# Performance work log

Measured on AMD Instinct MI355X. Metric: run time of the kernel, lower is better.

Reference implementation:

```python
import jax, jax.numpy as jnp
import numpy as np

ANGSTROM_TO_METER = 1e-10
COULOMB_CONSTANT = 8987551792.3
ELECTRON_CHARGE = 1.602176634e-19
EV_TO_JOULE = 1.602176634e-19
COUL_DAMPING_BETA = 18.7
R0_METER = 2.2 * ANGSTROM_TO_METER
EWALD_P = 0.3275911
EWALD_A = (0.254829592, -0.284496736, 1.421413741, -1.453152027, 1.061405429)
EWALD_F = 2.0

N_ATOMS = 200000
N_EDGES = 8000000
N_GRAPHS = 256


def setup_inputs() -> dict:
    key = jax.random.key(0)
    k1, k2, k3, k4, k5 = jax.random.split(key, 5)
    dij = jax.random.normal(k1, (N_EDGES, 3), dtype=jnp.float32)  # Angstrom
    pred_charge = jax.random.normal(k2, (N_ATOMS,), dtype=jnp.float32)  # e
    g_ewald = jnp.full((1,), 3.0e9, dtype=jnp.float32)  # 1/m (~0.3 1/A)
    row = jax.random.randint(k3, (N_EDGES,), 0, N_ATOMS)
    col = jax.random.randint(k4, (N_EDGES,), 0, N_ATOMS)
    batch = jnp.sort(jax.random.randint(k5, (N_ATOMS,), 0, N_GRAPHS))
    return {"dij": dij, "pred_charge": pred_charge, "g_ewald": g_ewald,
            "row": row, "col": col, "batch": batch}


def reference(dij, pred_charge, g_ewald, row, col, batch):
    n_atoms = pred_charge.shape[0]
    dij_m = dij * ANGSTROM_TO_METER                      # [E,3] meters
    rij = jnp.sqrt(jnp.sum(dij_m * dij_m, axis=-1))      # [E]
    q = pred_charge * ELECTRON_CHARGE                    # Coulombs
    prefactor = COULOMB_CONSTANT * q[row] * q[col] / rij
    # exponential short-range damping below r0
    damp = jnp.where(rij < R0_METER,
                     jnp.exp(-COUL_DAMPING_BETA * (R0_METER - rij) / R0_METER),
                     jnp.ones_like(rij))
    ecoul = 0.5 * prefactor * damp
    fcoul = prefactor * damp / rij
    # Ewald real-space correction via Abramowitz-Stegun erfc polynomial
    grij = g_ewald[0] * rij
    expm2 = jnp.exp(-grij * grij)
    t = 1.0 / (1.0 + EWALD_P * grij)
    a0, a1, a2, a3, a4 = EWALD_A
    erfc = t * (a0 + t * (a1 + t * (a2 + t * (a3 + t * a4)))) * expm2
    ecoul = ecoul + prefactor * (erfc - 1.0)
    fcoul = fcoul + prefactor * (erfc + EWALD_F * grij * expm2 - 1.0) / rij
    # per-edge force vector, converted J/m -> eV/A
    fij = dij_m * (fcoul / rij)[:, None]                 # [E,3]
    fij_ev = fij * ANGSTROM_TO_METER / EV_TO_JOULE
    ecoul_ev = ecoul / EV_TO_JOULE
    # scatter edge->atom (by row), then atom->molecule (by batch)
    e_atom = jax.ops.segment_sum(ecoul_ev, row, num_segments=n_atoms)
    coul_energy = jax.ops.segment_sum(e_atom, batch, num_segments=N_GRAPHS)
    force_row = jax.ops.segment_sum(fij_ev, row, num_segments=n_atoms)
    force_col = jax.ops.segment_sum(fij_ev, col, num_segments=n_atoms)
    coul_force = force_row - force_col
    return coul_energy, coul_force
```

## Files before the change

kernel.cpp:

```cpp
#include <hip/hip_runtime.h>
#include <hip/hip_fp16.h>

#define N_GRAPHS_C 256
#define CHUNK_LOG 12
#define CHUNK (1 << CHUNK_LOG)
#define MAXB 64
#define NSLICE 12
#define NSLICE_FB 10
#define TPA 256
#define TPBB 512
#define SD 64
#define PSTR (CHUNK + 8)
#define FP_SCALE 1024.0f
#define FP_INV   (1.0f / 1024.0f)

__device__ __forceinline__ void edge_math(
    float dx, float dy, float dz, float qr, float qc, float gA,
    float& fx, float& fy, float& fz, float& ecoul)
{
    const float KEV = (float)(8987551792.3 * 1.602176634e-9);
    float r2 = dx * dx + dy * dy + dz * dz;
    float inv_r = rsqrtf(r2);
    float rA = r2 * inv_r;

    float pref = KEV * qr * qc * inv_r;

    float damp = 1.0f;
    if (rA < 2.2f)
        damp = __expf(-18.7f * (2.2f - rA) * (1.0f / 2.2f));

    float grij = gA * rA;
    float expm2 = __expf(-grij * grij);
    float t = 1.0f / (1.0f + 0.3275911f * grij);
    float erfc = t * (0.254829592f +
                 t * (-0.284496736f +
                 t * (1.421413741f +
                 t * (-1.453152027f +
                 t * 1.061405429f)))) * expm2;

    ecoul = pref * (0.5f * damp + (erfc - 1.0f));
    float S = damp + erfc + 2.0f * grij * expm2 - 1.0f;
    float fs = pref * S * (inv_r * inv_r);
    fx = dx * fs; fy = dy * fs; fz = dz * fs;
}

__device__ __forceinline__ uint2 pack_rec(float fx, float fy, float fz, unsigned lid)
{
    uint2 u;
    u.x = __builtin_bit_cast(unsigned, __floats2half2_rn(fx, fy));
    u.y = (__builtin_bit_cast(unsigned, __floats2half2_rn(fz, 0.0f)) & 0xFFFFu) |
          (lid << 16);
    return u;
}

__device__ __forceinline__ void acc_rec(int* acc, unsigned w0, unsigned w1)
{
    float2 xy = __half22float2(__builtin_bit_cast(__half2, w0));
    float fz = __half2float(__builtin_bit_cast(__half2, w1).x);
    unsigned idx = w1 >> 16;
    atomicAdd(&acc[idx],            __float2int_rn(xy.x * FP_SCALE));
    atomicAdd(&acc[PSTR + idx],     __float2int_rn(xy.y * FP_SCALE));
    atomicAdd(&acc[2 * PSTR + idx], __float2int_rn(fz   * FP_SCALE));
}

__global__ __launch_bounds__(256) void prep_qg(
    const float* __restrict__ q, const int* __restrict__ batch,
    float2* __restrict__ qg, float* __restrict__ ovf, int n_atoms)
{
    int i = blockIdx.x * 256 + threadIdx.x;
    if (i < n_atoms) {
        qg[i] = make_float2(q[i], __int_as_float(batch[i]));
        ovf[3 * i + 0] = 0.f;
        ovf[3 * i + 1] = 0.f;
        ovf[3 * i + 2] = 0.f;
    }
}

__global__ __launch_bounds__(TPA) void passA(
    const float* __restrict__ dij, const float2* __restrict__ qg,
    const float* __restrict__ g_ewald,
    const int* __restrict__ row, const int* __restrict__ col,
    uint2* __restrict__ records, int cap,
    unsigned* __restrict__ cnt_table,
    float* __restrict__ e_part,
    float* __restrict__ ovf,
    int n_edges, int nb, int tile_g)
{
    __shared__ uint2    stage[MAXB][SD + 1];
    __shared__ unsigned scnt[MAXB];
    __shared__ unsigned cnt[MAXB];
    __shared__ float    e_graph[4 * N_GRAPHS_C];

    int tid  = threadIdx.x;
    int wid  = tid >> 6;
    int lane = tid & 63;
    if (tid < MAXB) { scnt[tid] = 0u; cnt[tid] = 0u; }
    for (int i = tid; i < 4 * N_GRAPHS_C; i += TPA) e_graph[i] = 0.f;
    __syncthreads();

    float* e_my = &e_graph[wid * N_GRAPHS_C];

    int n4 = n_edges >> 2;
    int gbase = blockIdx.x * tile_g;
    int g1 = min(gbase + tile_g, n4);
    int nph = tile_g / TPA;

    const int4* row4 = (const int4*)row;
    const int4* col4 = (const int4*)col;
    const float4* dij4 = (const float4*)dij;

    const float gA = g_ewald[0] * 1e-10f;
    size_t blk_base = (size_t)blockIdx.x * nb * cap;

    int4 r_cur = make_int4(0, 0, 0, 0), c_cur = make_int4(0, 0, 0, 0);
    float2 vr_cur[4], vc_cur[4];
    {
        int g = gbase + tid;
        if (g < g1) { r_cur = row4[g]; c_cur = col4[g]; }
        vr_cur[0] = qg[r_cur.x]; vc_cur[0] = qg[c_cur.x];
        vr_cur[1] = qg[r_cur.y]; vc_cur[1] = qg[c_cur.y];
        vr_cur[2] = qg[r_cur.z]; vc_cur[2] = qg[c_cur.z];
        vr_cur[3] = qg[r_cur.w]; vc_cur[3] = qg[c_cur.w];
    }

    for (int p = 0; p < nph; ++p) {
        int g = gbase + p * TPA + tid;

        int4 r_nxt = make_int4(0, 0, 0, 0), c_nxt = make_int4(0, 0, 0, 0);
        if (p + 1 < nph && g + TPA < g1) {
            r_nxt = row4[g + TPA]; c_nxt = col4[g + TPA];
        }

        if (g < g1) {
            float4 d0 = dij4[3 * g + 0];
            float4 d1 = dij4[3 * g + 1];
            float4 d2 = dij4[3 * g + 2];
            float ex[4] = {d0.x, d0.w, d1.z, d2.y};
            float ey[4] = {d0.y, d1.x, d1.w, d2.z};
            float ez[4] = {d0.z, d1.y, d2.x, d2.w};
            int rr[4] = {r_cur.x, r_cur.y, r_cur.z, r_cur.w};
            int cc[4] = {c_cur.x, c_cur.y, c_cur.z, c_cur.w};

            #pragma unroll
            for (int j = 0; j < 4; ++j) {
                int r = rr[j], c = cc[j];
                float fx, fy, fz, ec;
                edge_math(ex[j], ey[j], ez[j], vr_cur[j].x, vc_cur[j].x, gA,
                          fx, fy, fz, ec);

                atomicAdd(&e_my[__float_as_int(vr_cur[j].y)], ec);

                int br = r >> CHUNK_LOG, bc = c >> CHUNK_LOG;
                unsigned pr = atomicAdd(&scnt[br], 1u);
                unsigned pc = atomicAdd(&scnt[bc], 1u);
                if (pr < SD)
                    stage[br][pr] = pack_rec(fx, fy, fz, (unsigned)(r & (CHUNK - 1)));
                else {
                    atomicAdd(&ovf[3 * r + 0], fx);
                    atomicAdd(&ovf[3 * r + 1], fy);
                    atomicAdd(&ovf[3 * r + 2], fz);
                }
                if (pc < SD)
                    stage[bc][pc] = pack_rec(-fx, -fy, -fz, (unsigned)(c & (CHUNK - 1)));
                else {
                    atomicAdd(&ovf[3 * c + 0], -fx);
                    atomicAdd(&ovf[3 * c + 1], -fy);
                    atomicAdd(&ovf[3 * c + 2], -fz);
                }
            }
        }

        float2 vr_n[4], vc_n[4];
        vr_n[0] = qg[r_nxt.x]; vc_n[0] = qg[c_nxt.x];
        vr_n[1] = qg[r_nxt.y]; vc_n[1] = qg[c_nxt.y];
        vr_n[2] = qg[r_nxt.z]; vc_n[2] = qg[c_nxt.z];
        vr_n[3] = qg[r_nxt.w]; vc_n[3] = qg[c_nxt.w];

        __syncthreads();

        for (int b = wid; b < nb; b += TPA / 64) {
            unsigned m = min(scnt[b], (unsigned)SD);
            unsigned base = 0;
            if (lane == 0) base = atomicAdd(&cnt[b], m);
            base = (unsigned)__shfl((int)base, 0, 64);
            for (unsigned i = lane; i < m; i += 64) {
                uint2 rv = stage[b][i];
                unsigned slot = base + i;
                if (slot < (unsigned)cap) {
                    records[blk_base + (size_t)b * cap + slot] = rv;
                } else {
                    float2 xy = __half22float2(__builtin_bit_cast(__half2, rv.x));
                    float fzv = __half2float(__builtin_bit_cast(__half2, rv.y).x);
                    int atom = (b << CHUNK_LOG) + (int)(rv.y >> 16);
                    atomicAdd(&ovf[3 * atom + 0], xy.x);
                    atomicAdd(&ovf[3 * atom + 1], xy.y);
                    atomicAdd(&ovf[3 * atom + 2], fzv);
                }
            }
            if (lane == 0) scnt[b] = 0u;
        }
        __syncthreads();

        r_cur = r_nxt; c_cur = c_nxt;
        #pragma unroll
        for (int j = 0; j < 4; ++j) { vr_cur[j] = vr_n[j]; vc_cur[j] = vc_n[j]; }
    }

    if (tid < nb) cnt_table[(size_t)blockIdx.x * nb + tid] = min(cnt[tid], (unsigned)cap);
    for (int g2 = tid; g2 < N_GRAPHS_C; g2 += TPA)
        e_part[(size_t)blockIdx.x * N_GRAPHS_C + g2] =
            e_graph[g2] + e_graph[N_GRAPHS_C + g2] +
            e_graph[2 * N_GRAPHS_C + g2] + e_graph[3 * N_GRAPHS_C + g2];
}

__global__ __launch_bounds__(TPBB) void passB(
    const uint2* __restrict__ records, int cap,
    const unsigned* __restrict__ cnt_table,
    int* __restrict__ partial, int nblkA, int nb, int nslice)
{
    __shared__ int acc[3 * PSTR];

    int b = blockIdx.x / nslice;
    int s = blockIdx.x % nslice;
    int k0 = (int)((long long)s * nblkA / nslice);
    int k1 = (int)((long long)(s + 1) * nblkA / nslice);

    for (int i = threadIdx.x; i < 3 * PSTR; i += TPBB) acc[i] = 0;
    __syncthreads();

    int wid  = threadIdx.x >> 6;
    int lane = threadIdx.x & 63;
    const int W = TPBB / 64;

    for (int kb = k0 + wid; kb < k1; kb += 4 * W) {
        int ka = kb, kB = kb + W, kc = kb + 2 * W, kd = kb + 3 * W;
        bool e1 = kB < k1, e2 = kc < k1, e3 = kd < k1;

        unsigned n0 = cnt_table[(size_t)ka * nb + b];
        unsigned n1 = e1 ? cnt_table[(size_t)kB * nb + b] : 0u;
        unsigned n2 = e2 ? cnt_table[(size_t)kc * nb + b] : 0u;
        unsigned n3 = e3 ? cnt_table[(size_t)kd * nb + b] : 0u;

        const uint2* r0 = records + ((size_t)ka * nb + b) * cap;
        const uint2* r1 = e1 ? records + ((size_t)kB * nb + b) * cap : r0;
        const uint2* r2 = e2 ? records + ((size_t)kc * nb + b) * cap : r0;
        const uint2* r3 = e3 ? records + ((size_t)kd * nb + b) * cap : r0;
        const uint4* q0 = (const uint4*)r0;
        const uint4* q1 = (const uint4*)r1;
        const uint4* q2 = (const uint4*)r2;
        const uint4* q3 = (const uint4*)r3;

        unsigned h0 = n0 >> 1, h1 = n1 >> 1, h2 = n2 >> 1, h3 = n3 >> 1;
        unsigned hm = max(max(h0, h1), max(h2, h3));

        for (unsigned i = lane; i < hm; i += 64) {
            uint4 v0 = q0[h0 ? min(i, h0 - 1u) : 0u];
            uint4 v1 = q1[h1 ? min(i, h1 - 1u) : 0u];
            uint4 v2 = q2[h2 ? min(i, h2 - 1u) : 0u];
            uint4 v3 = q3[h3 ? min(i, h3 - 1u) : 0u];
            if (i < h0) { acc_rec(acc, v0.x, v0.y); acc_rec(acc, v0.z, v0.w); }
            if (i < h1) { acc_rec(acc, v1.x, v1.y); acc_rec(acc, v1.z, v1.w); }
            if (i < h2) { acc_rec(acc, v2.x, v2.y); acc_rec(acc, v2.z, v2.w); }
            if (i < h3) { acc_rec(acc, v3.x, v3.y); acc_rec(acc, v3.z, v3.w); }
        }
        if (lane == 0) {
            if (n0 & 1u) { uint2 t = r0[n0 - 1]; acc_rec(acc, t.x, t.y); }
            if (n1 & 1u) { uint2 t = r1[n1 - 1]; acc_rec(acc, t.x, t.y); }
            if (n2 & 1u) { uint2 t = r2[n2 - 1]; acc_rec(acc, t.x, t.y); }
            if (n3 & 1u) { uint2 t = r3[n3 - 1]; acc_rec(acc, t.x, t.y); }
        }
    }
    __syncthreads();

    int* dst = partial + (size_t)blockIdx.x * 3 * CHUNK;
    for (int i = threadIdx.x; i < 3 * CHUNK; i += TPBB) {
        int pl = i >> CHUNK_LOG;
        int ofs = i & (CHUNK - 1);
        dst[i] = acc[pl * PSTR + ofs];
    }
}

__global__ __launch_bounds__(256) void fin_force(
    const int* __restrict__ partial, const float* __restrict__ ovf,
    const float* __restrict__ e_part,
    float* __restrict__ force, float* __restrict__ energy,
    int n_atoms, int nslice, int nblkA, int nfblk)
{
    if ((int)blockIdx.x >= nfblk) {
        int g = (blockIdx.x - nfblk) * 4 + (threadIdx.x >> 6);
        int lane = threadIdx.x & 63;
        float s = 0.f;
        for (int k = lane; k < nblkA; k += 64)
            s += e_part[(size_t)k * N_GRAPHS_C + g];
        for (int off = 32; off > 0; off >>= 1) s += __shfl_down(s, off, 64);
        if (lane == 0) energy[g] = s;
        return;
    }
    int a = blockIdx.x * 256 + threadIdx.x;
    if (a >= n_atoms) return;
    int b = a >> CHUNK_LOG, l = a & (CHUNK - 1);
    long long sx = 0, sy = 0, sz = 0;
    const int* p = partial + (size_t)b * nslice * 3 * CHUNK + l;
    for (int s = 0; s < nslice; ++s) {
        const int* ps = p + (size_t)s * 3 * CHUNK;
        sx += ps[0]; sy += ps[CHUNK]; sz += ps[2 * CHUNK];
    }
    force[3 * a + 0] = ovf[3 * a + 0] + (float)sx * FP_INV;
    force[3 * a + 1] = ovf[3 * a + 1] + (float)sy * FP_INV;
    force[3 * a + 2] = ovf[3 * a + 2] + (float)sz * FP_INV;
}

__global__ __launch_bounds__(1024) void chunk_kernel(
    const float* __restrict__ dij, const float* __restrict__ q,
    const float* __restrict__ g_ewald,
    const int* __restrict__ row, const int* __restrict__ col,
    float* __restrict__ partial, int n_edges, int n_chunks, int n_slices)
{
    __shared__ float acc[CHUNK * 4];
    int c = blockIdx.x % n_chunks;
    int p = blockIdx.x / n_chunks;
    int cbase = c << CHUNK_LOG;
    for (int i = threadIdx.x; i < CHUNK * 4; i += 1024) acc[i] = 0.f;
    __syncthreads();
    const float gA = g_ewald[0] * 1e-10f;
    int n4 = (n_edges + 3) >> 2;
    int g0 = (int)((long long)p * n4 / n_slices);
    int g1 = (int)((long long)(p + 1) * n4 / n_slices);
    const int4* row4 = (const int4*)row;
    const int4* col4 = (const int4*)col;
    for (int g = g0 + threadIdx.x; g < g1; g += 1024) {
        int4 r4 = row4[g];
        int4 c4 = col4[g];
        int rr[4] = {r4.x, r4.y, r4.z, r4.w};
        int cc[4] = {c4.x, c4.y, c4.z, c4.w};
        #pragma unroll
        for (int j = 0; j < 4; ++j) {
            int e = 4 * g + j;
            if (e >= n_edges) break;
            int rl = rr[j] - cbase;
            int cl = cc[j] - cbase;
            bool hr = (unsigned)rl < (unsigned)CHUNK;
            bool hc = (unsigned)cl < (unsigned)CHUNK;
            if (!(hr || hc)) continue;
            float fx, fy, fz, ec;
            edge_math(dij[3 * e], dij[3 * e + 1], dij[3 * e + 2],
                      q[rr[j]], q[cc[j]], gA, fx, fy, fz, ec);
            if (hr) {
                atomicAdd(&acc[4 * rl + 0], fx);
                atomicAdd(&acc[4 * rl + 1], fy);
                atomicAdd(&acc[4 * rl + 2], fz);
                atomicAdd(&acc[4 * rl + 3], ec);
            }
            if (hc) {
                atomicAdd(&acc[4 * cl + 0], -fx);
                atomicAdd(&acc[4 * cl + 1], -fy);
                atomicAdd(&acc[4 * cl + 2], -fz);
            }
        }
    }
    __syncthreads();
    float4* dst = (float4*)partial + (size_t)(c * n_slices + p) * CHUNK;
    const float4* src = (const float4*)acc;
    for (int i = threadIdx.x; i < CHUNK; i += 1024) dst[i] = src[i];
}

__global__ __launch_bounds__(256) void finalize_kernel(
    const float* __restrict__ partial, const int* __restrict__ batch,
    float* __restrict__ energy, float* __restrict__ force,
    int n_atoms, int n_slices)
{
    int i = blockIdx.x * blockDim.x + threadIdx.x;
    float fx = 0.f, fy = 0.f, fz = 0.f, en = 0.f;
    if (i < n_atoms) {
        int c = i >> CHUNK_LOG;
        int l = i & (CHUNK - 1);
        const float4* base = (const float4*)partial + (size_t)c * n_slices * CHUNK + l;
        for (int p = 0; p < n_slices; ++p) {
            float4 v = base[(size_t)p * CHUNK];
            fx += v.x; fy += v.y; fz += v.z; en += v.w;
        }
        force[3 * i + 0] = fx;
        force[3 * i + 1] = fy;
        force[3 * i + 2] = fz;
    }
    int ic = i < n_atoms ? i : (n_atoms - 1);
    int b = batch[ic];
    float v = (i < n_atoms) ? en : 0.0f;
    int b0 = __shfl(b, 0, 64);
    unsigned long long m = __ballot(b == b0);
    if (m == ~0ull) {
        for (int off = 32; off > 0; off >>= 1)
            v += __shfl_down(v, off, 64);
        if ((threadIdx.x & 63) == 0) atomicAdd(&energy[b0], v);
    } else {
        atomicAdd(&energy[b], v);
    }
}

extern "C" void kernel_launch(void* const* d_in, const int* in_sizes, int n_in,
                              void* d_out, int out_size, void* d_ws, size_t ws_size,
                              hipStream_t stream) {
    const float* dij     = (const float*)d_in[0];
    const float* q       = (const float*)d_in[1];
    const float* g_ewald = (const float*)d_in[2];
    const int*   row     = (const int*)d_in[3];
    const int*   col     = (const int*)d_in[4];
    const int*   batch   = (const int*)d_in[5];

    int n_edges = in_sizes[0] / 3;
    int n_atoms = in_sizes[1];

    float* energy = (float*)d_out;
    float* force  = (float*)d_out + N_GRAPHS_C;

    int nb = (n_atoms + CHUNK - 1) >> CHUNK_LOG;
    int n4 = n_edges >> 2;

    size_t sz_partial = (size_t)nb * NSLICE * 3 * CHUNK * sizeof(int);
    size_t sz_ovf     = (size_t)3 * n_atoms * sizeof(float);
    size_t sz_qg      = (size_t)n_atoms * sizeof(float2);

    const int  tile_sel[2]   = {1024, 2048};
    const int  mincap_sel[2] = {224, 416};
    const int  capmax_sel[2] = {256, 512};

    int tile_g = 0, cap = 0, nblkA = 0;
    size_t sz_epart = 0, sz_cnt = 0;
    for (int t = 0; t < 2 && tile_g == 0; ++t) {
        int nba = (n4 + tile_sel[t] - 1) / tile_sel[t];
        size_t se = (size_t)nba * N_GRAPHS_C * sizeof(float);
        size_t sc = (size_t)nba * nb * sizeof(unsigned);
        size_t fixed = ((sz_partial + 255) & ~(size_t)255) +
                       ((se         + 255) & ~(size_t)255) +
                       ((sc         + 255) & ~(size_t)255) +
                       ((sz_ovf     + 255) & ~(size_t)255) +
                       ((sz_qg      + 255) & ~(size_t)255) + 512;
        if ((long long)ws_size > (long long)fixed) {
            long long c = ((long long)ws_size - (long long)fixed) /
                          ((long long)nba * nb * 8);
            c = (c / 32) * 32;
            if (c > capmax_sel[t]) c = capmax_sel[t];
            if (c >= mincap_sel[t]) {
                tile_g = tile_sel[t]; cap = (int)c; nblkA = nba;
                sz_epart = se; sz_cnt = sc;
            }
        }
    }

    bool fast = (nb <= MAXB) && ((n_edges & 3) == 0) && (tile_g > 0) &&
                ((tile_g % TPA) == 0);

    if (fast) {
        char* ws = (char*)d_ws;
        size_t off = 0;
        uint2*    records  = (uint2*)(ws + off);
        off += (size_t)nblkA * nb * cap * 8;   off = (off + 255) & ~(size_t)255;
        int*      partial  = (int*)(ws + off);
        off += sz_partial;                     off = (off + 255) & ~(size_t)255;
        float*    e_part   = (float*)(ws + off);
        off += sz_epart;                       off = (off + 255) & ~(size_t)255;
        unsigned* cnt_tab  = (unsigned*)(ws + off);
        off += sz_cnt;                         off = (off + 255) & ~(size_t)255;
        float*    ovf      = (float*)(ws + off);
        off += sz_ovf;                         off = (off + 255) & ~(size_t)255;
        float2*   qg       = (float2*)(ws + off);

        prep_qg<<<(n_atoms + 255) / 256, 256, 0, stream>>>(q, batch, qg, ovf, n_atoms);

        passA<<<nblkA, TPA, 0, stream>>>(
            dij, qg, g_ewald, row, col,
            records, cap, cnt_tab, e_part, ovf, n_edges, nb, tile_g);

        passB<<<nb * NSLICE, TPBB, 0, stream>>>(
            records, cap, cnt_tab, partial, nblkA, nb, NSLICE);

        int nfblk = (n_atoms + 255) / 256;
        fin_force<<<nfblk + N_GRAPHS_C / 4, 256, 0, stream>>>(
            partial, ovf, e_part, force, energy, n_atoms, NSLICE, nblkA, nfblk);
    } else {
        size_t need_chunk = (size_t)nb * NSLICE_FB * CHUNK * 4 * sizeof(float);
        if (ws_size >= need_chunk) {
            hipMemsetAsync(d_out, 0, N_GRAPHS_C * sizeof(float), stream);
            chunk_kernel<<<nb * NSLICE_FB, 1024, 0, stream>>>(
                dij, q, g_ewald, row, col, (float*)d_ws, n_edges, nb, NSLICE_FB);
            finalize_kernel<<<(n_atoms + 255) / 256, 256, 0, stream>>>(
                (const float*)d_ws, batch, energy, force, n_atoms, NSLICE_FB);
        }
    }
}
```

Before: 343.3 us.

## Atomically merge passB slices into per-atom totals and repad passA staging

passB no longer writes one partial fixed-point buffer per slice. Each block now atomically adds its nonzero shared-memory sums directly into a per-atom integer array, so fin_force reads a single value per component instead of summing over twelve slices. passB is also widened to 1024 threads. The passA staging buffer is rewritten as a flat u32 array with an odd stride to change the LDS bank pattern. The change trades global partial-buffer traffic and the final reduction for global atomic contention and a larger workspace zeroing step in prep_qg.

```diff
diff --git a/kernel.cpp b/kernel.cpp
--- a/kernel.cpp
+++ b/kernel.cpp
@@ -8,8 +8,9 @@
 #define NSLICE 12
 #define NSLICE_FB 10
 #define TPA 256
-#define TPBB 512
+#define TPBB 1024
 #define SD 64
+#define SSTR (2 * SD + 1)
 #define PSTR (CHUNK + 8)
 #define FP_SCALE 1024.0f
 #define FP_INV   (1.0f / 1024.0f)
@@ -65,7 +66,8 @@
 
 __global__ __launch_bounds__(256) void prep_qg(
     const float* __restrict__ q, const int* __restrict__ batch,
-    float2* __restrict__ qg, float* __restrict__ ovf, int n_atoms)
+    float2* __restrict__ qg, float* __restrict__ ovf, int* __restrict__ fint,
+    int n_atoms)
 {
     int i = blockIdx.x * 256 + threadIdx.x;
     if (i < n_atoms) {
@@ -73,6 +75,9 @@
         ovf[3 * i + 0] = 0.f;
         ovf[3 * i + 1] = 0.f;
         ovf[3 * i + 2] = 0.f;
+        fint[i] = 0;
+        fint[n_atoms + i] = 0;
+        fint[2 * n_atoms + i] = 0;
     }
 }
 
@@ -86,7 +91,7 @@
     float* __restrict__ ovf,
     int n_edges, int nb, int tile_g)
 {
-    __shared__ uint2    stage[MAXB][SD + 1];
+    __shared__ unsigned stageU[MAXB * SSTR];
     __shared__ unsigned scnt[MAXB];
     __shared__ unsigned cnt[MAXB];
     __shared__ float    e_graph[4 * N_GRAPHS_C];
@@ -153,16 +158,20 @@
                 int br = r >> CHUNK_LOG, bc = c >> CHUNK_LOG;
                 unsigned pr = atomicAdd(&scnt[br], 1u);
                 unsigned pc = atomicAdd(&scnt[bc], 1u);
-                if (pr < SD)
-                    stage[br][pr] = pack_rec(fx, fy, fz, (unsigned)(r & (CHUNK - 1)));
-                else {
+                if (pr < SD) {
+                    uint2 rv = pack_rec(fx, fy, fz, (unsigned)(r & (CHUNK - 1)));
+                    int bi = br * SSTR + 2 * (int)pr;
+                    stageU[bi] = rv.x; stageU[bi + 1] = rv.y;
+                } else {
                     atomicAdd(&ovf[3 * r + 0], fx);
                     atomicAdd(&ovf[3 * r + 1], fy);
                     atomicAdd(&ovf[3 * r + 2], fz);
                 }
-                if (pc < SD)
-                    stage[bc][pc] = pack_rec(-fx, -fy, -fz, (unsigned)(c & (CHUNK - 1)));
-                else {
+                if (pc < SD) {
+                    uint2 rv = pack_rec(-fx, -fy, -fz, (unsigned)(c & (CHUNK - 1)));
+                    int bi = bc * SSTR + 2 * (int)pc;
+                    stageU[bi] = rv.x; stageU[bi + 1] = rv.y;
+                } else {
                     atomicAdd(&ovf[3 * c + 0], -fx);
                     atomicAdd(&ovf[3 * c + 1], -fy);
                     atomicAdd(&ovf[3 * c + 2], -fz);
@@ -183,8 +192,9 @@
             unsigned base = 0;
             if (lane == 0) base = atomicAdd(&cnt[b], m);
             base = (unsigned)__shfl((int)base, 0, 64);
+            int sb = b * SSTR;
             for (unsigned i = lane; i < m; i += 64) {
-                uint2 rv = stage[b][i];
+                uint2 rv = make_uint2(stageU[sb + 2 * i], stageU[sb + 2 * i + 1]);
                 unsigned slot = base + i;
                 if (slot < (unsigned)cap) {
                     records[blk_base + (size_t)b * cap + slot] = rv;
@@ -216,7 +226,7 @@
 __global__ __launch_bounds__(TPBB) void passB(
     const uint2* __restrict__ records, int cap,
     const unsigned* __restrict__ cnt_table,
-    int* __restrict__ partial, int nblkA, int nb, int nslice)
+    int* __restrict__ fint, int nblkA, int nb, int nslice, int n_atoms)
 {
     __shared__ int acc[3 * PSTR];
 
@@ -272,19 +282,22 @@
     }
     __syncthreads();
 
-    int* dst = partial + (size_t)blockIdx.x * 3 * CHUNK;
+    int abase = b << CHUNK_LOG;
     for (int i = threadIdx.x; i < 3 * CHUNK; i += TPBB) {
-        int pl = i >> CHUNK_LOG;
+        int pl  = i >> CHUNK_LOG;
         int ofs = i & (CHUNK - 1);
-        dst[i] = acc[pl * PSTR + ofs];
+        int v = acc[pl * PSTR + ofs];
+        int a = abase + ofs;
+        if (v != 0 && a < n_atoms)
+            atomicAdd(&fint[pl * n_atoms + a], v);
     }
 }
 
 __global__ __launch_bounds__(256) void fin_force(
-    const int* __restrict__ partial, const float* __restrict__ ovf,
+    const int* __restrict__ fint, const float* __restrict__ ovf,
     const float* __restrict__ e_part,
     float* __restrict__ force, float* __restrict__ energy,
-    int n_atoms, int nslice, int nblkA, int nfblk)
+    int n_atoms, int nblkA, int nfblk)
 {
     if ((int)blockIdx.x >= nfblk) {
         int g = (blockIdx.x - nfblk) * 4 + (threadIdx.x >> 6);
@@ -298,16 +311,9 @@
     }
     int a = blockIdx.x * 256 + threadIdx.x;
     if (a >= n_atoms) return;
-    int b = a >> CHUNK_LOG, l = a & (CHUNK - 1);
-    long long sx = 0, sy = 0, sz = 0;
-    const int* p = partial + (size_t)b * nslice * 3 * CHUNK + l;
-    for (int s = 0; s < nslice; ++s) {
-        const int* ps = p + (size_t)s * 3 * CHUNK;
-        sx += ps[0]; sy += ps[CHUNK]; sz += ps[2 * CHUNK];
-    }
-    force[3 * a + 0] = ovf[3 * a + 0] + (float)sx * FP_INV;
-    force[3 * a + 1] = ovf[3 * a + 1] + (float)sy * FP_INV;
-    force[3 * a + 2] = ovf[3 * a + 2] + (float)sz * FP_INV;
+    force[3 * a + 0] = ovf[3 * a + 0] + (float)fint[a] * FP_INV;
+    force[3 * a + 1] = ovf[3 * a + 1] + (float)fint[n_atoms + a] * FP_INV;
+    force[3 * a + 2] = ovf[3 * a + 2] + (float)fint[2 * n_atoms + a] * FP_INV;
 }
 
 __global__ __launch_bounds__(1024) void chunk_kernel(
@@ -416,7 +422,7 @@
     int nb = (n_atoms + CHUNK - 1) >> CHUNK_LOG;
     int n4 = n_edges >> 2;
 
-    size_t sz_partial = (size_t)nb * NSLICE * 3 * CHUNK * sizeof(int);
+    size_t sz_fint    = (size_t)3 * n_atoms * sizeof(int);
     size_t sz_ovf     = (size_t)3 * n_atoms * sizeof(float);
     size_t sz_qg      = (size_t)n_atoms * sizeof(float2);
 
@@ -430,11 +436,11 @@
         int nba = (n4 + tile_sel[t] - 1) / tile_sel[t];
         size_t se = (size_t)nba * N_GRAPHS_C * sizeof(float);
         size_t sc = (size_t)nba * nb * sizeof(unsigned);
-        size_t fixed = ((sz_partial + 255) & ~(size_t)255) +
-                       ((se         + 255) & ~(size_t)255) +
-                       ((sc         + 255) & ~(size_t)255) +
-                       ((sz_ovf     + 255) & ~(size_t)255) +
-                       ((sz_qg      + 255) & ~(size_t)255) + 512;
+        size_t fixed = ((sz_fint + 255) & ~(size_t)255) +
+                       ((se      + 255) & ~(size_t)255) +
+                       ((sc      + 255) & ~(size_t)255) +
+                       ((sz_ovf  + 255) & ~(size_t)255) +
+                       ((sz_qg   + 255) & ~(size_t)255) + 512;
         if ((long long)ws_size > (long long)fixed) {
             long long c = ((long long)ws_size - (long long)fixed) /
                           ((long long)nba * nb * 8);
@@ -455,8 +461,8 @@
         size_t off = 0;
         uint2*    records  = (uint2*)(ws + off);
         off += (size_t)nblkA * nb * cap * 8;   off = (off + 255) & ~(size_t)255;
-        int*      partial  = (int*)(ws + off);
-        off += sz_partial;                     off = (off + 255) & ~(size_t)255;
+        int*      fint     = (int*)(ws + off);
+        off += sz_fint;                        off = (off + 255) & ~(size_t)255;
         float*    e_part   = (float*)(ws + off);
         off += sz_epart;                       off = (off + 255) & ~(size_t)255;
         unsigned* cnt_tab  = (unsigned*)(ws + off);
@@ -465,18 +471,19 @@
         off += sz_ovf;                         off = (off + 255) & ~(size_t)255;
         float2*   qg       = (float2*)(ws + off);
 
-        prep_qg<<<(n_atoms + 255) / 256, 256, 0, stream>>>(q, batch, qg, ovf, n_atoms);
+        prep_qg<<<(n_atoms + 255) / 256, 256, 0, stream>>>(
+            q, batch, qg, ovf, fint, n_atoms);
 
         passA<<<nblkA, TPA, 0, stream>>>(
             dij, qg, g_ewald, row, col,
             records, cap, cnt_tab, e_part, ovf, n_edges, nb, tile_g);
 
         passB<<<nb * NSLICE, TPBB, 0, stream>>>(
-            records, cap, cnt_tab, partial, nblkA, nb, NSLICE);
+            records, cap, cnt_tab, fint, nblkA, nb, NSLICE, n_atoms);
 
         int nfblk = (n_atoms + 255) / 256;
         fin_force<<<nfblk + N_GRAPHS_C / 4, 256, 0, stream>>>(
-            partial, ovf, e_part, force, energy, n_atoms, NSLICE, nblkA, nfblk);
+            fint, ovf, e_part, force, energy, n_atoms, nblkA, nfblk);
     } else {
         size_t need_chunk = (size_t)nb * NSLICE_FB * CHUNK * 4 * sizeof(float);
         if (ws_size >= need_chunk) {
```

New measurement: 347.0 us. No clear change (+1.1%).
